# Kernel tuning notes

Hardware: AMD Instinct MI355X
Metric: run time of the kernel (lower is better)

## Reference

```python
import jax, jax.numpy as jnp
import numpy as np

D_MODEL = 1024
NUM_HEADS = 16
D_K = D_MODEL // NUM_HEADS
D_FF = 4096
EPS = 1e-5


def _layernorm(x, gamma, beta):
    mu = jnp.mean(x, axis=-1, keepdims=True)
    var = jnp.mean(jnp.square(x - mu), axis=-1, keepdims=True)
    return (x - mu) * jax.lax.rsqrt(var + EPS) * gamma + beta


def setup_inputs() -> dict:
    key = jax.random.key(0)
    ks = jax.random.split(key, 16)
    B, S = 4, 2048
    s_in = 1.0 / np.sqrt(D_MODEL)
    s_ff = 1.0 / np.sqrt(D_FF)
    inp = {
        "x": jax.random.normal(ks[0], (B, S, D_MODEL), jnp.float32),
        "src_mask": jnp.ones((B, 1, 1, S), jnp.int32),
        "w_q": jax.random.normal(ks[1], (D_MODEL, D_MODEL), jnp.float32) * s_in,
        "b_q": jnp.zeros((D_MODEL,), jnp.float32),
        "w_k": jax.random.normal(ks[2], (D_MODEL, D_MODEL), jnp.float32) * s_in,
        "b_k": jnp.zeros((D_MODEL,), jnp.float32),
        "w_v": jax.random.normal(ks[3], (D_MODEL, D_MODEL), jnp.float32) * s_in,
        "b_v": jnp.zeros((D_MODEL,), jnp.float32),
        "w_o": jax.random.normal(ks[4], (D_MODEL, D_MODEL), jnp.float32) * s_in,
        "b_o": jnp.zeros((D_MODEL,), jnp.float32),
        "w1": jax.random.normal(ks[5], (D_MODEL, D_FF), jnp.float32) * s_in,
        "b1": jnp.zeros((D_FF,), jnp.float32),
        "w2": jax.random.normal(ks[6], (D_FF, D_MODEL), jnp.float32) * s_ff,
        "b2": jnp.zeros((D_MODEL,), jnp.float32),
        "g1": jnp.ones((D_MODEL,), jnp.float32),
        "be1": jnp.zeros((D_MODEL,), jnp.float32),
        "g2": jnp.ones((D_MODEL,), jnp.float32),
        "be2": jnp.zeros((D_MODEL,), jnp.float32),
    }
    return inp


def reference(x, src_mask, w_q, b_q, w_k, b_k, w_v, b_v, w_o, b_o,
              w1, b1, w2, b2, g1, be1, g2, be2):
    B, S, _ = x.shape

    def split_heads(t):  # [B,S,D] -> [B,H,S,dk]
        return t.reshape(B, S, NUM_HEADS, D_K).transpose(0, 2, 1, 3)

    q = split_heads(x @ w_q + b_q)
    k = split_heads(x @ w_k + b_k)
    v = split_heads(x @ w_v + b_v)

    scores = jnp.einsum("bhqd,bhkd->bhqk", q, k) / np.sqrt(D_K)
    scores = jnp.where(src_mask == 0, -jnp.inf, scores)
    attn = jax.nn.softmax(scores, axis=-1)
    ctx = jnp.einsum("bhqk,bhkd->bhqd", attn, v)
    merged = ctx.transpose(0, 2, 1, 3).reshape(B, S, D_MODEL)
    attn_out = merged @ w_o + b_o

    h = _layernorm(x + attn_out, g1, be1)
    ff = jax.nn.relu(h @ w1 + b1) @ w2 + b2
    return _layernorm(h + ff, g2, be2)
```

## Files before the change

### kernel.cpp

```cpp
#include <hip/hip_runtime.h>

typedef unsigned short u16;
typedef __attribute__((ext_vector_type(4))) unsigned short u16x4;
typedef __attribute__((ext_vector_type(8))) short bf16x8;
typedef __attribute__((ext_vector_type(4))) float f32x4;
typedef __attribute__((ext_vector_type(16))) float f32x16;

__device__ inline float bf2f(u16 u) {
  union { unsigned int i; float f; } v; v.i = ((unsigned int)u) << 16; return v.f;
}
__device__ inline u16 f2bf(float f) {
  union { float f; unsigned int i; } v; v.f = f;
  unsigned int r = v.i + 0x7fffu + ((v.i >> 16) & 1u);
  return (u16)(r >> 16);
}
__device__ inline unsigned int cvt_pk_bf16(float lo, float hi) {
  unsigned int r;
  asm("v_cvt_pk_bf16_f32 %0, %1, %2" : "=v"(r) : "v"(lo), "v"(hi));
  return r;
}
__device__ inline f32x16 zero16() {
  f32x16 z;
  #pragma unroll
  for (int i = 0; i < 16; ++i) z[i] = 0.f;
  return z;
}

typedef const __attribute__((address_space(1))) unsigned int* gas_t;
typedef __attribute__((address_space(3))) unsigned int* las_t;
__device__ inline void gload_lds16(const u16* g, u16* l) {
  __builtin_amdgcn_global_load_lds((gas_t)(unsigned long long)(const void*)g,
                                   (las_t)(unsigned int)(unsigned long long)(void*)l,
                                   16, 0, 0);
}

__global__ __launch_bounds__(256) void cvt_bf16(const float* __restrict__ src,
                                                u16* __restrict__ dst, int n) {
  int i = (blockIdx.x * 256 + threadIdx.x) * 4;
  if (i >= n) return;
  float4 v = *(const float4*)(src + i);
  u16x4 o;
  o.x = f2bf(v.x); o.y = f2bf(v.y); o.z = f2bf(v.z); o.w = f2bf(v.w);
  *(u16x4*)(dst + i) = o;
}

__global__ __launch_bounds__(256) void concat3(const float* __restrict__ a,
                                               const float* __restrict__ b,
                                               const float* __restrict__ c,
                                               float* __restrict__ o, int n) {
  int i = blockIdx.x * 256 + threadIdx.x;
  if (i >= n) return;
  o[i] = a[i]; o[n + i] = b[i]; o[2 * n + i] = c[i];
}

__global__ __launch_bounds__(256) void transpose_f32_bf16(const float* __restrict__ src,
                                                          u16* __restrict__ dst,
                                                          int R, int C) {
  __shared__ u16 tile[32][33];
  int tx = threadIdx.x & 31, ty = threadIdx.x >> 5;
  int c0 = blockIdx.x * 32, r0 = blockIdx.y * 32;
  #pragma unroll
  for (int i = ty; i < 32; i += 8)
    tile[i][tx] = f2bf(src[(size_t)(r0 + i) * C + c0 + tx]);
  __syncthreads();
  #pragma unroll
  for (int i = ty; i < 32; i += 8)
    dst[(size_t)(c0 + i) * R + r0 + tx] = tile[tx][i];
}

__global__ __launch_bounds__(256) void transpose_v(const u16* __restrict__ src,
                                                   u16* __restrict__ VT,
                                                   int B, int S, int H, int RS, int CO) {
  __shared__ u16 tile[32][33];
  int tx = threadIdx.x & 31, ty = threadIdx.x >> 5;
  int s0 = blockIdx.x * 32, d0 = blockIdx.y * 32;
  int bh = blockIdx.z;
  int b = bh / H, h = bh % H;
  #pragma unroll
  for (int i = ty; i < 32; i += 8)
    tile[i][tx] = src[(size_t)(b * S + s0 + i) * RS + CO + h * 64 + d0 + tx];
  __syncthreads();
  #pragma unroll
  for (int i = ty; i < 32; i += 8)
    VT[((size_t)bh * 64 + d0 + i) * S + s0 + tx] = tile[tx][i];
}

__global__ __launch_bounds__(256) void gemm_bt(const u16* __restrict__ A,
                                               const u16* __restrict__ Bt,
                                               const float* __restrict__ bias,
                                               u16* __restrict__ C,
                                               int M, int N, int K, int relu) {
  __shared__ u16 As[128 * 64];
  __shared__ u16 Bs[128 * 64];
  const int tid = threadIdx.x;
  const int lane = tid & 63, wid = tid >> 6;
  const int lr = lane & 15, quad = lane >> 4;
  const int wm = (wid >> 1) * 64, wn = (wid & 1) * 64;
  const int m0 = blockIdx.y * 128, n0 = blockIdx.x * 128;
  const int grow = lane >> 3;
  const int gcol = ((lane & 7) ^ grow) * 8;
  const int rsw = (lr & 7) << 3;

  f32x4 acc[4][4];
  const f32x4 zero = {0.f, 0.f, 0.f, 0.f};
  #pragma unroll
  for (int mt = 0; mt < 4; ++mt)
    #pragma unroll
    for (int nt = 0; nt < 4; ++nt) acc[mt][nt] = zero;

  for (int k0 = 0; k0 < K; k0 += 64) {
    #pragma unroll
    for (int it = 0; it < 4; ++it) {
      int rbase = wid * 32 + it * 8;
      gload_lds16(A + (size_t)(m0 + rbase + grow) * K + k0 + gcol, &As[rbase * 64]);
      gload_lds16(Bt + (size_t)(n0 + rbase + grow) * K + k0 + gcol, &Bs[rbase * 64]);
    }
    __syncthreads();
    #pragma unroll
    for (int kk = 0; kk < 2; ++kk) {
      bf16x8 af[4], bfr[4];
      #pragma unroll
      for (int mt = 0; mt < 4; ++mt)
        af[mt] = *(const bf16x8*)(&As[(wm + mt * 16 + lr) * 64 + ((kk * 32 + quad * 8) ^ rsw)]);
      #pragma unroll
      for (int nt = 0; nt < 4; ++nt)
        bfr[nt] = *(const bf16x8*)(&Bs[(wn + nt * 16 + lr) * 64 + ((kk * 32 + quad * 8) ^ rsw)]);
      #pragma unroll
      for (int mt = 0; mt < 4; ++mt)
        #pragma unroll
        for (int nt = 0; nt < 4; ++nt)
          acc[mt][nt] = __builtin_amdgcn_mfma_f32_16x16x32_bf16(af[mt], bfr[nt], acc[mt][nt], 0, 0, 0);
    }
    __syncthreads();
  }

  #pragma unroll
  for (int nt = 0; nt < 4; ++nt) {
    int n = n0 + wn + nt * 16 + lr;
    float bv = bias[n];
    #pragma unroll
    for (int mt = 0; mt < 4; ++mt) {
      #pragma unroll
      for (int i = 0; i < 4; ++i) {
        int m = m0 + wm + mt * 16 + quad * 4 + i;
        float v = acc[mt][nt][i] + bv;
        if (relu) v = fmaxf(v, 0.f);
        C[(size_t)m * N + n] = f2bf(v);
      }
    }
  }
}

__global__ __launch_bounds__(128) void flash_attn(const u16* __restrict__ Qp,
                                                  const u16* __restrict__ Kp,
                                                  const u16* __restrict__ VT,
                                                  const int* __restrict__ mask,
                                                  u16* __restrict__ ctx,
                                                  int B, int S, int H, int QSTR) {
  __shared__ u16 kt_lds[64 * 64];
  __shared__ u16 vt_lds[64 * 64];
  const int tid = threadIdx.x;
  const int lane = tid & 63, wid = tid >> 6;
  const int l31 = lane & 31, hi = lane >> 5;
  const int bh = blockIdx.y;
  const int qb = blockIdx.x;
  const int b = bh / H, h = bh % H;
  const u16* vt_base = VT + (size_t)bh * 64 * S;
  const int* mbase = mask + b * S;
  const float SC = 0.125f * 1.44269504089f;

  const int srl = lane >> 3;
  const int scol = ((lane & 7) ^ srl) * 8;
  const int rsw = (lane & 7) << 3;

  const int q = qb * 64 + wid * 32 + l31;
  bf16x8 qf[4];
  {
    const u16* qptr = Qp + (size_t)(b * S + q) * QSTR + h * 64;
    #pragma unroll
    for (int t = 0; t < 4; ++t)
      qf[t] = *(const bf16x8*)(qptr + t * 16 + hi * 8);
  }

  float m_i = -1e30f, l_i = 0.f;
  f32x16 o0 = zero16(), o1 = zero16();

  const u16* kgp = Kp + ((size_t)b * S + wid * 32 + srl) * QSTR + h * 64 + scol;
  const u16* vgp = vt_base + (size_t)(wid * 32 + srl) * S + scol;
  u16* klb = &kt_lds[(wid * 32) * 64];
  u16* vlb = &vt_lds[(wid * 32) * 64];

  for (int kt = 0; kt < S; kt += 64) {
    #pragma unroll
    for (int it = 0; it < 4; ++it) {
      gload_lds16(kgp + (size_t)(kt + it * 8) * QSTR, klb + it * 8 * 64);
      gload_lds16(vgp + (size_t)(it * 8) * S + kt, vlb + it * 8 * 64);
    }
    int mv = mbase[kt + lane];
    unsigned long long bal = __ballot(mv != 0);
    __syncthreads();

    f32x16 sa0 = zero16(), sa1 = zero16();
    const u16* krow0 = &kt_lds[l31 * 64];
    const u16* krow1 = &kt_lds[(32 + l31) * 64];
    __builtin_amdgcn_s_setprio(1);
    #pragma unroll
    for (int dblock = 0; dblock < 4; ++dblock) {
      int c = (dblock * 16 + hi * 8) ^ rsw;
      bf16x8 kf0 = *(const bf16x8*)(krow0 + c);
      bf16x8 kf1 = *(const bf16x8*)(krow1 + c);
      sa0 = __builtin_amdgcn_mfma_f32_32x32x16_bf16(kf0, qf[dblock], sa0, 0, 0, 0);
      sa1 = __builtin_amdgcn_mfma_f32_32x32x16_bf16(kf1, qf[dblock], sa1, 0, 0, 0);
    }
    __builtin_amdgcn_s_setprio(0);

    if (bal != 0xFFFFFFFFFFFFFFFFull) {
      unsigned long long balh = bal >> (hi * 4);
      #pragma unroll
      for (int r = 0; r < 16; ++r) {
        int kloc = (r & 3) + 8 * (r >> 2);
        if (!((balh >> kloc) & 1)) sa0[r] = -2e30f;
        if (!((balh >> (32 + kloc)) & 1)) sa1[r] = -2e30f;
      }
    }

    float tmax = sa0[0];
    #pragma unroll
    for (int r = 1; r < 16; ++r) tmax = fmaxf(tmax, sa0[r]);
    #pragma unroll
    for (int r = 0; r < 16; ++r) tmax = fmaxf(tmax, sa1[r]);
    tmax = fmaxf(tmax, __shfl_xor(tmax, 32, 64));
    if (__any(tmax > m_i + 44.0f)) {
      float mn = fmaxf(m_i, tmax);
      float al = exp2f((m_i - mn) * SC);
      m_i = mn;
      l_i *= al;
      #pragma unroll
      for (int r = 0; r < 16; ++r) { o0[r] *= al; o1[r] *= al; }
    }
    float msc = m_i * SC;
    float rs = 0.f;
    #pragma unroll
    for (int r = 0; r < 16; ++r) {
      float p0 = exp2f(__builtin_fmaf(sa0[r], SC, -msc));
      float p1 = exp2f(__builtin_fmaf(sa1[r], SC, -msc));
      sa0[r] = p0; sa1[r] = p1; rs += p0 + p1;
    }
    l_i += rs;

    unsigned pfw[4][4];
    #pragma unroll
    for (int b1 = 0; b1 < 2; ++b1) {
      #pragma unroll
      for (int pair = 0; pair < 2; ++pair) {
        unsigned X0 = cvt_pk_bf16(sa0[(2 * b1) * 4 + pair * 2], sa0[(2 * b1) * 4 + pair * 2 + 1]);
        unsigned Y0 = cvt_pk_bf16(sa0[(2 * b1 + 1) * 4 + pair * 2], sa0[(2 * b1 + 1) * 4 + pair * 2 + 1]);
        unsigned Xp0 = __shfl_xor(X0, 32, 64);
        unsigned Yp0 = __shfl_xor(Y0, 32, 64);
        pfw[b1][pair] = hi ? Yp0 : X0;
        pfw[b1][pair + 2] = hi ? Y0 : Xp0;
        unsigned X1 = cvt_pk_bf16(sa1[(2 * b1) * 4 + pair * 2], sa1[(2 * b1) * 4 + pair * 2 + 1]);
        unsigned Y1 = cvt_pk_bf16(sa1[(2 * b1 + 1) * 4 + pair * 2], sa1[(2 * b1 + 1) * 4 + pair * 2 + 1]);
        unsigned Xp1 = __shfl_xor(X1, 32, 64);
        unsigned Yp1 = __shfl_xor(Y1, 32, 64);
        pfw[2 + b1][pair] = hi ? Yp1 : X1;
        pfw[2 + b1][pair + 2] = hi ? Y1 : Xp1;
      }
    }

    const u16* vrow0 = &vt_lds[l31 * 64];
    const u16* vrow1 = &vt_lds[(32 + l31) * 64];
    __builtin_amdgcn_s_setprio(1);
    #pragma unroll
    for (int kb = 0; kb < 4; ++kb) {
      int c = (kb * 16 + hi * 8) ^ rsw;
      bf16x8 vf0 = *(const bf16x8*)(vrow0 + c);
      bf16x8 vf1 = *(const bf16x8*)(vrow1 + c);
      union { unsigned w[4]; bf16x8 v; } pu;
      pu.w[0] = pfw[kb][0]; pu.w[1] = pfw[kb][1];
      pu.w[2] = pfw[kb][2]; pu.w[3] = pfw[kb][3];
      o0 = __builtin_amdgcn_mfma_f32_32x32x16_bf16(vf0, pu.v, o0, 0, 0, 0);
      o1 = __builtin_amdgcn_mfma_f32_32x32x16_bf16(vf1, pu.v, o1, 0, 0, 0);
    }
    __builtin_amdgcn_s_setprio(0);
    __syncthreads();
  }

  l_i += __shfl_xor(l_i, 32, 64);
  float linv = 1.f / fmaxf(l_i, 1e-30f);
  u16* op = ctx + (size_t)(b * S + q) * (H * 64) + h * 64;
  #pragma unroll
  for (int rq = 0; rq < 4; ++rq) {
    uint2 w0, w1;
    w0.x = cvt_pk_bf16(o0[rq * 4 + 0] * linv, o0[rq * 4 + 1] * linv);
    w0.y = cvt_pk_bf16(o0[rq * 4 + 2] * linv, o0[rq * 4 + 3] * linv);
    *(uint2*)(op + rq * 8 + hi * 4) = w0;
    w1.x = cvt_pk_bf16(o1[rq * 4 + 0] * linv, o1[rq * 4 + 1] * linv);
    w1.y = cvt_pk_bf16(o1[rq * 4 + 2] * linv, o1[rq * 4 + 3] * linv);
    *(uint2*)(op + 32 + rq * 8 + hi * 4) = w1;
  }
}

__device__ inline float block_reduce_sum(float v, float* sbuf) {
  #pragma unroll
  for (int m = 1; m < 64; m <<= 1) v += __shfl_xor(v, m, 64);
  int w = threadIdx.x >> 6;
  if ((threadIdx.x & 63) == 0) sbuf[w] = v;
  __syncthreads();
  v = sbuf[0] + sbuf[1] + sbuf[2] + sbuf[3];
  __syncthreads();
  return v;
}

__global__ __launch_bounds__(256) void add_ln(const float* __restrict__ a32,
                                              const u16* __restrict__ a16,
                                              const u16* __restrict__ b,
                                              const float* __restrict__ g,
                                              const float* __restrict__ be,
                                              u16* __restrict__ out16,
                                              float* __restrict__ out32, int D) {
  __shared__ float sbuf[4];
  int row = blockIdx.x;
  size_t base = (size_t)row * D;
  int i = threadIdx.x * 4;
  float v[4];
  {
    u16x4 bv = *(const u16x4*)(b + base + i);
    if (a32) {
      float4 av = *(const float4*)(a32 + base + i);
      v[0] = av.x + bf2f(bv.x); v[1] = av.y + bf2f(bv.y);
      v[2] = av.z + bf2f(bv.z); v[3] = av.w + bf2f(bv.w);
    } else {
      u16x4 av = *(const u16x4*)(a16 + base + i);
      v[0] = bf2f(av.x) + bf2f(bv.x); v[1] = bf2f(av.y) + bf2f(bv.y);
      v[2] = bf2f(av.z) + bf2f(bv.z); v[3] = bf2f(av.w) + bf2f(bv.w);
    }
  }
  float sum = v[0] + v[1] + v[2] + v[3];
  sum = block_reduce_sum(sum, sbuf);
  float mean = sum / (float)D;
  float var = 0.f;
  #pragma unroll
  for (int j = 0; j < 4; ++j) { float d = v[j] - mean; var += d * d; }
  var = block_reduce_sum(var, sbuf);
  float rstd = rsqrtf(var / (float)D + 1e-5f);
  float4 gv = *(const float4*)(g + i);
  float4 bev = *(const float4*)(be + i);
  float o0 = (v[0] - mean) * rstd * gv.x + bev.x;
  float o1 = (v[1] - mean) * rstd * gv.y + bev.y;
  float o2 = (v[2] - mean) * rstd * gv.z + bev.z;
  float o3 = (v[3] - mean) * rstd * gv.w + bev.w;
  if (out32) {
    float4 o = {o0, o1, o2, o3};
    *(float4*)(out32 + base + i) = o;
  } else {
    u16x4 o;
    o.x = f2bf(o0); o.y = f2bf(o1); o.z = f2bf(o2); o.w = f2bf(o3);
    *(u16x4*)(out16 + base + i) = o;
  }
}

extern "C" void kernel_launch(void* const* d_in, const int* in_sizes, int n_in,
                              void* d_out, int out_size, void* d_ws, size_t ws_size,
                              hipStream_t stream) {
  (void)in_sizes; (void)n_in; (void)out_size; (void)ws_size;
  const float* x   = (const float*)d_in[0];
  const int* mask  = (const int*)d_in[1];
  const float* wq  = (const float*)d_in[2];
  const float* bq  = (const float*)d_in[3];
  const float* wk  = (const float*)d_in[4];
  const float* bk  = (const float*)d_in[5];
  const float* wv  = (const float*)d_in[6];
  const float* bv  = (const float*)d_in[7];
  const float* wo  = (const float*)d_in[8];
  const float* bo  = (const float*)d_in[9];
  const float* w1  = (const float*)d_in[10];
  const float* b1  = (const float*)d_in[11];
  const float* w2  = (const float*)d_in[12];
  const float* b2  = (const float*)d_in[13];
  const float* g1  = (const float*)d_in[14];
  const float* be1 = (const float*)d_in[15];
  const float* g2  = (const float*)d_in[16];
  const float* be2 = (const float*)d_in[17];

  const int B = 4, S = 2048, D = 1024, H = 16, DFF = 4096;
  const int D3 = 3 * D;
  const size_t TOK = (size_t)B * S;
  const size_t TD = TOK * D;

  u16* ws   = (u16*)d_ws;
  u16* QKVp = ws;
  u16* xb   = ws + 3 * TD;
  u16* VT   = xb;
  u16* CTX  = ws + 4 * TD;
  u16* ATT  = ws + 5 * TD;
  u16* Hb   = ws + 6 * TD;
  u16* QKVT = ws + 7 * TD;
  u16* WOT  = QKVT + 3 * (size_t)D * D;
  u16* W1T  = WOT + (size_t)D * D;
  u16* FF1  = ws;
  u16* FF2  = ATT;
  u16* W2T  = QKVT;
  float* biasc = (float*)CTX;

  dim3 blk(256);

  cvt_bf16<<<dim3((unsigned)(TD / (256 * 4))), blk, 0, stream>>>(x, xb, (int)TD);
  concat3<<<dim3(4), blk, 0, stream>>>(bq, bk, bv, biasc, D);

  transpose_f32_bf16<<<dim3(D / 32, D / 32), blk, 0, stream>>>(wq, QKVT, D, D);
  transpose_f32_bf16<<<dim3(D / 32, D / 32), blk, 0, stream>>>(wk, QKVT + (size_t)D * D, D, D);
  transpose_f32_bf16<<<dim3(D / 32, D / 32), blk, 0, stream>>>(wv, QKVT + 2 * (size_t)D * D, D, D);
  transpose_f32_bf16<<<dim3(D / 32, D / 32), blk, 0, stream>>>(wo, WOT, D, D);
  transpose_f32_bf16<<<dim3(DFF / 32, D / 32), blk, 0, stream>>>(w1, W1T, D, DFF);

  gemm_bt<<<dim3(D3 / 128, TOK / 128), blk, 0, stream>>>(xb, QKVT, biasc, QKVp, (int)TOK, D3, D, 0);

  transpose_v<<<dim3(S / 32, 2, B * H), blk, 0, stream>>>(QKVp, VT, B, S, H, D3, 2 * D);

  flash_attn<<<dim3(S / 64, B * H), dim3(128), 0, stream>>>(
      QKVp, QKVp + D, VT, mask, CTX, B, S, H, D3);

  gemm_bt<<<dim3(D / 128, TOK / 128), blk, 0, stream>>>(CTX, WOT, bo, ATT, (int)TOK, D, D, 0);

  transpose_f32_bf16<<<dim3(D / 32, DFF / 32), blk, 0, stream>>>(w2, W2T, DFF, D);

  add_ln<<<dim3((unsigned)TOK), blk, 0, stream>>>(x, (const u16*)nullptr, ATT, g1, be1,
                                                  Hb, (float*)nullptr, D);

  gemm_bt<<<dim3(DFF / 128, TOK / 128), blk, 0, stream>>>(Hb, W1T, b1, FF1, (int)TOK, DFF, D, 1);
  gemm_bt<<<dim3(D / 128, TOK / 128), blk, 0, stream>>>(FF1, W2T, b2, FF2, (int)TOK, D, DFF, 0);

  add_ln<<<dim3((unsigned)TOK), blk, 0, stream>>>((const float*)nullptr, Hb, FF2, g2, be2,
                                                  (u16*)nullptr, (float*)d_out, D);
}
```

Measured before the change: 642.8 us.

## Add 256x256 pipelined GEMM for QKV/FFN1 and widen flash-attn blocks to 4 waves

```diff
diff --git a/kernel.cpp b/kernel.cpp
--- a/kernel.cpp
+++ b/kernel.cpp
@@ -151,7 +151,118 @@
   }
 }
 
-__global__ __launch_bounds__(128) void flash_attn(const u16* __restrict__ Qp,
+__global__ __launch_bounds__(512, 2) void gemm256(const u16* __restrict__ A,
+                                                  const u16* __restrict__ Bt,
+                                                  const float* __restrict__ bias,
+                                                  u16* __restrict__ C,
+                                                  int M, int N, int K, int relu) {
+  __shared__ u16 As[2][256][64];
+  __shared__ u16 Bs[2][256][64];
+  const int tid = threadIdx.x;
+  const int lane = tid & 63, wid = tid >> 6;
+  const int lr = lane & 15, quad = lane >> 4;
+  const int wm2 = wid >> 2, wn4 = wid & 3;
+  const int m0 = blockIdx.y * 256, n0 = blockIdx.x * 256;
+  const int srl = lane >> 3;
+  const int scol = ((lane & 7) ^ srl) * 8;
+  const int rsw = (lr & 7) << 3;
+  const int NT = K >> 6;
+
+  f32x4 acc[8][4];
+  #pragma unroll
+  for (int mi = 0; mi < 8; ++mi)
+    #pragma unroll
+    for (int ni = 0; ni < 4; ++ni) {
+      acc[mi][ni][0] = 0.f; acc[mi][ni][1] = 0.f;
+      acc[mi][ni][2] = 0.f; acc[mi][ni][3] = 0.f;
+    }
+
+#define STAGE_A(TT, MQ)                                                        \
+  if ((TT) < NT) {                                                             \
+    int c2 = (TT) & 1, k0s = (TT) << 6;                                        \
+    const u16* ga = A + (size_t)(m0 + (MQ) * 64 + wid * 8 + srl) * K + k0s + scol; \
+    gload_lds16(ga, &As[c2][(MQ) * 64 + wid * 8][0]);                          \
+    gload_lds16(ga + (size_t)128 * K, &As[c2][128 + (MQ) * 64 + wid * 8][0]);  \
+  }
+#define STAGE_B(TT, HH)                                                        \
+  if ((TT) < NT) {                                                             \
+    int c2 = (TT) & 1, k0s = (TT) << 6;                                        \
+    const u16* gb = Bt + (size_t)(n0 + (HH) * 128 + wid * 8 + srl) * K + k0s + scol; \
+    gload_lds16(gb, &Bs[c2][(HH) * 128 + wid * 8][0]);                         \
+    gload_lds16(gb + (size_t)64 * K, &Bs[c2][(HH) * 128 + 64 + wid * 8][0]);   \
+  }
+
+#define PHASE(MQ, NQ, STAGE_STMT)                                              \
+  {                                                                            \
+    bf16x8 af[4][2], bfr[2][2];                                                \
+    _Pragma("unroll")                                                          \
+    for (int mt = 0; mt < 4; ++mt)                                             \
+      _Pragma("unroll")                                                        \
+      for (int kk = 0; kk < 2; ++kk)                                           \
+        af[mt][kk] = *(const bf16x8*)(&As[c][wm2 * 128 + (MQ) * 64 + mt * 16 + lr] \
+                                         [(kk * 32 + quad * 8) ^ rsw]);        \
+    _Pragma("unroll")                                                          \
+    for (int nt = 0; nt < 2; ++nt)                                             \
+      _Pragma("unroll")                                                        \
+      for (int kk = 0; kk < 2; ++kk)                                           \
+        bfr[nt][kk] = *(const bf16x8*)(&Bs[c][wn4 * 64 + (NQ) * 32 + nt * 16 + lr] \
+                                          [(kk * 32 + quad * 8) ^ rsw]);       \
+    STAGE_STMT;                                                                \
+    __builtin_amdgcn_s_barrier();                                              \
+    __builtin_amdgcn_s_setprio(1);                                             \
+    _Pragma("unroll")                                                          \
+    for (int mt = 0; mt < 4; ++mt)                                             \
+      _Pragma("unroll")                                                        \
+      for (int nt = 0; nt < 2; ++nt)                                           \
+        _Pragma("unroll")                                                      \
+        for (int kk = 0; kk < 2; ++kk)                                         \
+          acc[(MQ) * 4 + mt][(NQ) * 2 + nt] = __builtin_amdgcn_mfma_f32_16x16x32_bf16( \
+              af[mt][kk], bfr[nt][kk], acc[(MQ) * 4 + mt][(NQ) * 2 + nt], 0, 0, 0); \
+    __builtin_amdgcn_s_setprio(0);                                             \
+    __builtin_amdgcn_s_barrier();                                              \
+  }
+
+  STAGE_A(0, 0);
+  STAGE_A(0, 1);
+  STAGE_B(0, 0);
+  STAGE_B(0, 1);
+  STAGE_A(1, 0);
+
+  for (int t = 0; t < NT; ++t) {
+    const int c = t & 1;
+    if (t + 1 < NT) {
+      asm volatile("s_waitcnt vmcnt(2)" ::: "memory");
+    } else {
+      asm volatile("s_waitcnt vmcnt(0)" ::: "memory");
+    }
+    __builtin_amdgcn_s_barrier();
+    PHASE(0, 0, STAGE_A(t + 1, 1));
+    PHASE(0, 1, STAGE_B(t + 1, 0));
+    PHASE(1, 0, STAGE_B(t + 1, 1));
+    PHASE(1, 1, STAGE_A(t + 2, 0));
+  }
+#undef PHASE
+#undef STAGE_A
+#undef STAGE_B
+
+  #pragma unroll
+  for (int ni = 0; ni < 4; ++ni) {
+    int n = n0 + wn4 * 64 + ni * 16 + lr;
+    float bv = bias[n];
+    #pragma unroll
+    for (int mi = 0; mi < 8; ++mi) {
+      #pragma unroll
+      for (int i = 0; i < 4; ++i) {
+        int m = m0 + wm2 * 128 + mi * 16 + quad * 4 + i;
+        float v = acc[mi][ni][i] + bv;
+        if (relu) v = fmaxf(v, 0.f);
+        C[(size_t)m * N + n] = f2bf(v);
+      }
+    }
+  }
+}
+
+__global__ __launch_bounds__(256) void flash_attn(const u16* __restrict__ Qp,
                                                   const u16* __restrict__ Kp,
                                                   const u16* __restrict__ VT,
                                                   const int* __restrict__ mask,
@@ -163,7 +274,6 @@
   const int lane = tid & 63, wid = tid >> 6;
   const int l31 = lane & 31, hi = lane >> 5;
   const int bh = blockIdx.y;
-  const int qb = blockIdx.x;
   const int b = bh / H, h = bh % H;
   const u16* vt_base = VT + (size_t)bh * 64 * S;
   const int* mbase = mask + b * S;
@@ -173,7 +283,7 @@
   const int scol = ((lane & 7) ^ srl) * 8;
   const int rsw = (lane & 7) << 3;
 
-  const int q = qb * 64 + wid * 32 + l31;
+  const int q = blockIdx.x * 128 + wid * 32 + l31;
   bf16x8 qf[4];
   {
     const u16* qptr = Qp + (size_t)(b * S + q) * QSTR + h * 64;
@@ -185,17 +295,16 @@
   float m_i = -1e30f, l_i = 0.f;
   f32x16 o0 = zero16(), o1 = zero16();
 
-  const u16* kgp = Kp + ((size_t)b * S + wid * 32 + srl) * QSTR + h * 64 + scol;
-  const u16* vgp = vt_base + (size_t)(wid * 32 + srl) * S + scol;
-  u16* klb = &kt_lds[(wid * 32) * 64];
-  u16* vlb = &vt_lds[(wid * 32) * 64];
+  const u16* kgp = Kp + ((size_t)b * S + wid * 16 + srl) * QSTR + h * 64 + scol;
+  const u16* vgp = vt_base + (size_t)(wid * 16 + srl) * S + scol;
+  u16* klb = &kt_lds[(wid * 16) * 64];
+  u16* vlb = &vt_lds[(wid * 16) * 64];
 
   for (int kt = 0; kt < S; kt += 64) {
-    #pragma unroll
-    for (int it = 0; it < 4; ++it) {
-      gload_lds16(kgp + (size_t)(kt + it * 8) * QSTR, klb + it * 8 * 64);
-      gload_lds16(vgp + (size_t)(it * 8) * S + kt, vlb + it * 8 * 64);
-    }
+    gload_lds16(kgp + (size_t)kt * QSTR, klb);
+    gload_lds16(kgp + (size_t)(kt + 8) * QSTR, klb + 8 * 64);
+    gload_lds16(vgp + kt, vlb);
+    gload_lds16(vgp + 8 * (size_t)S + kt, vlb + 8 * 64);
     int mv = mbase[kt + lane];
     unsigned long long bal = __ballot(mv != 0);
     __syncthreads();
@@ -414,11 +523,12 @@
   transpose_f32_bf16<<<dim3(D / 32, D / 32), blk, 0, stream>>>(wo, WOT, D, D);
   transpose_f32_bf16<<<dim3(DFF / 32, D / 32), blk, 0, stream>>>(w1, W1T, D, DFF);
 
-  gemm_bt<<<dim3(D3 / 128, TOK / 128), blk, 0, stream>>>(xb, QKVT, biasc, QKVp, (int)TOK, D3, D, 0);
+  gemm256<<<dim3(D3 / 256, TOK / 256), dim3(512), 0, stream>>>(
+      xb, QKVT, biasc, QKVp, (int)TOK, D3, D, 0);
 
   transpose_v<<<dim3(S / 32, 2, B * H), blk, 0, stream>>>(QKVp, VT, B, S, H, D3, 2 * D);
 
-  flash_attn<<<dim3(S / 64, B * H), dim3(128), 0, stream>>>(
+  flash_attn<<<dim3(S / 128, B * H), blk, 0, stream>>>(
       QKVp, QKVp + D, VT, mask, CTX, B, S, H, D3);
 
   gemm_bt<<<dim3(D / 128, TOK / 128), blk, 0, stream>>>(CTX, WOT, bo, ATT, (int)TOK, D, D, 0);
@@ -428,7 +538,8 @@
   add_ln<<<dim3((unsigned)TOK), blk, 0, stream>>>(x, (const u16*)nullptr, ATT, g1, be1,
                                                   Hb, (float*)nullptr, D);
 
-  gemm_bt<<<dim3(DFF / 128, TOK / 128), blk, 0, stream>>>(Hb, W1T, b1, FF1, (int)TOK, DFF, D, 1);
+  gemm256<<<dim3(DFF / 256, TOK / 256), dim3(512), 0, stream>>>(
+      Hb, W1T, b1, FF1, (int)TOK, DFF, D, 1);
   gemm_bt<<<dim3(D / 128, TOK / 128), blk, 0, stream>>>(FF1, W2T, b2, FF2, (int)TOK, D, DFF, 0);
 
   add_ln<<<dim3((unsigned)TOK), blk, 0, stream>>>((const float*)nullptr, Hb, FF2, g2, be2,
```

After: 626.6 us. 1.03x faster.
